# Performance work log

Hardware: AMD Instinct MI355X
Metric: run time of the kernel (lower is better)

## Reference

```python
import jax, jax.numpy as jnp
import numpy as np

NUM_HEADS = 4
KEY_DIM = 64
D_MODEL = 256
OUTPUT_DIM = 256


def setup_inputs() -> dict:
    key = jax.random.key(0)
    ks = jax.random.split(key, 11)
    B, T, D = 16, 1024, D_MODEL
    HD = NUM_HEADS * KEY_DIM
    s = 0.02
    return {
        "query": jax.random.normal(ks[0], (B, T, D), jnp.float32),
        "key": jax.random.normal(ks[1], (B, T, D), jnp.float32),
        "value": jax.random.normal(ks[2], (B, T, D), jnp.float32),
        "Wq": jax.random.normal(ks[3], (D, HD), jnp.float32) * s,
        "bq": jnp.zeros((HD,), jnp.float32),
        "Wk": jax.random.normal(ks[4], (D, HD), jnp.float32) * s,
        "bk": jnp.zeros((HD,), jnp.float32),
        "Wv": jax.random.normal(ks[5], (D, KEY_DIM), jnp.float32) * s,
        "bv": jnp.zeros((KEY_DIM,), jnp.float32),
        "Wo": jax.random.normal(ks[6], (HD, OUTPUT_DIM), jnp.float32) * s,
        "bo": jnp.zeros((OUTPUT_DIM,), jnp.float32),
    }


def reference(query, key, value, Wq, bq, Wk, bk, Wv, bv, Wo, bo):
    B, Tq, _ = query.shape
    Tk = key.shape[1]
    H, Dk = NUM_HEADS, KEY_DIM
    # projections
    q = (query @ Wq + bq).reshape(B, Tq, H, Dk)  # [B,Tq,H,Dk]
    k = (key @ Wk + bk).reshape(B, Tk, H, Dk)    # [B,Tk,H,Dk]
    v = value @ Wv + bv                           # [B,Tk,Dk] shared across heads
    scale = jnp.asarray(Dk, q.dtype) ** -0.5
    # scores [B,H,Tq,Tk]
    score = jnp.einsum("bqhd,bkhd->bhqk", q, k) * scale
    attn = jax.nn.softmax(score, axis=-1)
    # broadcast-V attention: [B,H,Tq,Tk] x [B,Tk,Dk] -> [B,H,Tq,Dk]
    out = jnp.einsum("bhqk,bkd->bhqd", attn, v)
    out = out.transpose(0, 2, 1, 3).reshape(B, Tq, H * Dk)
    return out @ Wo + bo
```

## Files before the change

### kernel.cpp

```cpp
#include <hip/hip_runtime.h>
#include <hip/hip_bf16.h>


typedef __attribute__((ext_vector_type(8))) short short8;
typedef __attribute__((ext_vector_type(4))) short s16x4;
typedef __attribute__((ext_vector_type(4))) float f32x4;

__device__ __forceinline__ short f2bf(float x) {
    return __builtin_bit_cast(short, __float2bfloat16(x));
}

__device__ __forceinline__ float exp2_fast(float x) {
#if __has_builtin(__builtin_amdgcn_exp2f)
    return __builtin_amdgcn_exp2f(x);
#else
    float r; asm("v_exp_f32 %0, %1" : "=v"(r) : "v"(x)); return r;
#endif
}

__device__ __forceinline__ f32x4 mfma16(short8 a, short8 b, f32x4 c) {
    return __builtin_amdgcn_mfma_f32_16x16x32_bf16(a, b, c, 0, 0, 0);
}
__device__ __forceinline__ f32x4 mfma16k16(s16x4 a, s16x4 b, f32x4 c) {
    return __builtin_amdgcn_mfma_f32_16x16x16bf16_1k(a, b, c, 0, 0, 0);
}

__device__ __forceinline__ void gll16(const float4* gsrc, float4* ldst) {
    __builtin_amdgcn_global_load_lds(
        (const __attribute__((address_space(1))) void*)gsrc,
        (__attribute__((address_space(3))) void*)ldst, 16, 0, 0);
}

#define QSCALE 0.18033688011112042f

__global__ void prep_weights(const float* __restrict__ Wq, const float* __restrict__ Wk,
                             const float* __restrict__ Wv, const float* __restrict__ Wo,
                             short* __restrict__ WqtF, short* __restrict__ WktF,
                             short* __restrict__ WvtF, short* __restrict__ WotF) {
    int tid = blockIdx.x * 256 + threadIdx.x;
    int n = tid >> 8, k = tid & 255;
    int off = ((n >> 6) << 14) + (((n >> 4) & 3) << 12) + ((k >> 5) << 9)
            + (((k >> 3) & 3) << 7) + ((n & 15) << 3) + (k & 7);
    WqtF[off] = f2bf(Wq[k * 256 + n] * QSCALE);
    WktF[off] = f2bf(Wk[k * 256 + n]);
    WotF[off] = f2bf(Wo[k * 256 + n]);
    if (n < 64) {
        int offv = ((n >> 4) << 12) + ((k >> 5) << 9) + (((k >> 3) & 3) << 7)
                 + ((n & 15) << 3) + (k & 7);
        WvtF[offv] = f2bf(Wv[k * 64 + n]);
    }
}

__global__ __launch_bounds__(256) void proj_all(
        const float* __restrict__ query, const float* __restrict__ key_,
        const float* __restrict__ value,
        const short* __restrict__ WqtF, const short* __restrict__ WktF,
        const short* __restrict__ WvtF,
        const float* __restrict__ bq, const float* __restrict__ bk,
        const float* __restrict__ bv,
        short* __restrict__ qf, short* __restrict__ kf, short* __restrict__ vf) {
    __shared__ short At[16384];
    const int tid = threadIdx.x;
    const int lane = tid & 63, wave = tid >> 6;
    const int u = lane >> 4, r16 = lane & 15;
    const int m0 = blockIdx.x * 64;
    const int task = blockIdx.y;

    const float* A = task == 0 ? query : (task == 1 ? key_ : value);

    #pragma unroll
    for (int j = 0; j < 8; ++j) {
        int p8 = j * 4 + u;
        int row = (wave << 4) + r16;
        const float* src = A + (m0 + row) * 256 + p8 * 8;
        float4 a0 = *(const float4*)src;
        float4 a1 = *(const float4*)(src + 4);
        short8 w;
        w[0] = f2bf(a0.x); w[1] = f2bf(a0.y); w[2] = f2bf(a0.z); w[3] = f2bf(a0.w);
        w[4] = f2bf(a1.x); w[5] = f2bf(a1.y); w[6] = f2bf(a1.z); w[7] = f2bf(a1.w);
        int dst = ((p8 >> 2) << 11) + (wave << 9) + ((p8 & 3) << 7) + (r16 << 3);
        *(short8*)&At[dst] = w;
    }
    __syncthreads();

    const int b = m0 >> 10, t64 = (m0 & 1023) >> 6;

    if (task < 2) {
        const short* WtF = task == 0 ? WqtF : WktF;
        const float* bias = task == 0 ? bq : bk;
        const float bscale = task == 0 ? QSCALE : 1.0f;
        short* outF = task == 0 ? qf : kf;

        f32x4 acc[4][4] = {};
        const short* wb = WtF + (wave << 14);
        #pragma unroll
        for (int kk = 0; kk < 8; ++kk) {
            short8 af[4], bf8[4];
            #pragma unroll
            for (int f = 0; f < 4; ++f) af[f] = *(const short8*)&At[(kk << 11) + (f << 9) + lane * 8];
            #pragma unroll
            for (int g = 0; g < 4; ++g) bf8[g] = *(const short8*)&wb[(g << 12) + (kk << 9) + lane * 8];
            #pragma unroll
            for (int f = 0; f < 4; ++f)
                #pragma unroll
                for (int g = 0; g < 4; ++g)
                    acc[f][g] = mfma16(af[f], bf8[g], acc[f][g]);
        }

        float bvv[4];
        #pragma unroll
        for (int g = 0; g < 4; ++g) bvv[g] = bias[(wave << 6) + 16 * g + r16] * bscale;
        short* ob = outF + ((((b << 2) + wave) << 4) + t64) * 4096;
        #pragma unroll
        for (int f = 0; f < 4; ++f)
            #pragma unroll
            for (int g = 0; g < 4; ++g) {
                int base = (f << 10) + ((g >> 1) << 9)
                         + (((2 * g + (r16 >> 3)) & 3) << 7) + (r16 & 7);
                #pragma unroll
                for (int rr = 0; rr < 4; ++rr)
                    ob[base + (4 * u + rr) * 8] = f2bf(acc[f][g][rr] + bvv[g]);
            }
    } else {
        f32x4 acc[4] = {};
        #pragma unroll
        for (int kk = 0; kk < 8; ++kk) {
            short8 af = *(const short8*)&At[(kk << 11) + (wave << 9) + lane * 8];
            #pragma unroll
            for (int g = 0; g < 4; ++g) {
                short8 bf8 = *(const short8*)&WvtF[(g << 12) + (kk << 9) + lane * 8];
                acc[g] = mfma16(af, bf8, acc[g]);
            }
        }
        short* ob = vf + ((b << 4) + t64) * 4096;
        #pragma unroll
        for (int dg = 0; dg < 4; ++dg) {
            float bvv = bv[16 * dg + r16];
            s16x4 o;
            #pragma unroll
            for (int rr = 0; rr < 4; ++rr) o[rr] = f2bf(acc[dg][rr] + bvv);
            *(s16x4*)&ob[(dg << 10) + ((wave >> 1) << 9) + lane * 8 + ((wave & 1) << 2)] = o;
        }
    }
}

__global__ __launch_bounds__(256) void attn_kernel(const short* __restrict__ qF,
        const short* __restrict__ kF, const short* __restrict__ vF,
        short* __restrict__ aoF) {
    __shared__ float4 Kt[2][512];
    __shared__ float4 Vt[2][512];
    const int tid = threadIdx.x;
    const int lane = tid & 63, wave = tid >> 6;
    const int u = lane >> 4, r16 = lane & 15;

    const int lin = blockIdx.x;
    const int L = (lin & 7) * 64 + (lin >> 3);
    const int qt2 = L & 7, h = (L >> 3) & 3, b = L >> 5;

    const short* qb = qF + ((((b << 2) + h) << 4) + 2 * qt2) * 4096 + (wave << 10);
    short8 qA0 = *(const short8*)&qb[lane * 8];
    short8 qA1 = *(const short8*)&qb[512 + lane * 8];
    short8 qB0 = *(const short8*)&qb[4096 + lane * 8];
    short8 qB1 = *(const short8*)&qb[4096 + 512 + lane * 8];

    const float4* kb = (const float4*)(kF + (((b << 2) + h) << 16));
    const float4* vb = (const float4*)(vF + (b << 16));

    #pragma unroll
    for (int j = 0; j < 4; ++j) {
        int ch = (wave << 2) + j;
        if (ch < 8) gll16(kb + (ch << 6) + lane, (float4*)Kt[0] + (ch << 6));
        else        gll16(vb + ((ch - 8) << 6) + lane, (float4*)Vt[0] + ((ch - 8) << 6));
    }
    asm volatile("s_waitcnt vmcnt(0)" ::: "memory");
    __syncthreads();

    f32x4 acc0[4] = {}, acc1[4] = {};
    f32x4 accl0 = {}, accl1 = {};
    s16x4 ones;
    { short o = (short)0x3F80; ones[0] = o; ones[1] = o; ones[2] = o; ones[3] = o; }

    for (int kt = 0; kt < 16; ++kt) {
        const int buf = kt & 1;
        if (kt < 15) {
            const float4* ks = kb + (kt + 1) * 512;
            const float4* vs = vb + (kt + 1) * 512;
            float4* kd = (float4*)Kt[buf ^ 1];
            float4* vd = (float4*)Vt[buf ^ 1];
            #pragma unroll
            for (int j = 0; j < 4; ++j) {
                int ch = (wave << 2) + j;
                if (ch < 8) gll16(ks + (ch << 6) + lane, kd + (ch << 6));
                else        gll16(vs + ((ch - 8) << 6) + lane, vd + ((ch - 8) << 6));
            }
        }

        const short* Kl = (const short*)Kt[buf];
        const short* Vl = (const short*)Vt[buf];

        f32x4 s0[4], s1[4];
        __builtin_amdgcn_s_setprio(1);
        #pragma unroll
        for (int g = 0; g < 4; ++g) {
            short8 k0 = *(const short8*)&Kl[(g << 10) + lane * 8];
            short8 k1 = *(const short8*)&Kl[(g << 10) + 512 + lane * 8];
            f32x4 z0 = {}, z1 = {};
            z0 = mfma16(k0, qA0, z0);
            s0[g] = mfma16(k1, qA1, z0);
            z1 = mfma16(k0, qB0, z1);
            s1[g] = mfma16(k1, qB1, z1);
        }
        __builtin_amdgcn_s_setprio(0);

        s16x4 pk0[4], pk1[4];
        #pragma unroll
        for (int g = 0; g < 4; ++g)
            #pragma unroll
            for (int rr = 0; rr < 4; ++rr) {
                pk0[g][rr] = f2bf(exp2_fast(s0[g][rr]));
                pk1[g][rr] = f2bf(exp2_fast(s1[g][rr]));
            }

        __builtin_amdgcn_s_setprio(1);
        #pragma unroll
        for (int g = 0; g < 4; ++g) {
            accl0 = mfma16k16(ones, pk0[g], accl0);
            accl1 = mfma16k16(ones, pk1[g], accl1);
        }
        #pragma unroll
        for (int dg = 0; dg < 4; ++dg) {
            #pragma unroll
            for (int gp = 0; gp < 2; ++gp) {
                short8 v8 = *(const short8*)&Vl[(dg << 10) + (gp << 9) + lane * 8];
                s16x4 vlo = { v8[0], v8[1], v8[2], v8[3] };
                s16x4 vhi = { v8[4], v8[5], v8[6], v8[7] };
                acc0[dg] = mfma16k16(vlo, pk0[2 * gp], acc0[dg]);
                acc0[dg] = mfma16k16(vhi, pk0[2 * gp + 1], acc0[dg]);
                acc1[dg] = mfma16k16(vlo, pk1[2 * gp], acc1[dg]);
                acc1[dg] = mfma16k16(vhi, pk1[2 * gp + 1], acc1[dg]);
            }
        }
        __builtin_amdgcn_s_setprio(0);

        asm volatile("s_waitcnt vmcnt(0)" ::: "memory");
        __syncthreads();
    }

    float li0 = 1.0f / accl0[0];
    float li1 = 1.0f / accl1[0];

    short* ob0 = aoF + (((b << 4) + 2 * qt2) << 14);
    #pragma unroll
    for (int dg = 0; dg < 4; ++dg) {
        int off = ((2 * h + (dg >> 1)) << 11) + (wave << 9)
                + (((2 * dg + (u >> 1)) & 3) << 7) + (r16 << 3) + ((u & 1) << 2);
        s16x4 o0, o1;
        #pragma unroll
        for (int rr = 0; rr < 4; ++rr) {
            o0[rr] = f2bf(acc0[dg][rr] * li0);
            o1[rr] = f2bf(acc1[dg][rr] * li1);
        }
        *(s16x4*)&ob0[off] = o0;
        *(s16x4*)&ob0[16384 + off] = o1;
    }
}

__global__ __launch_bounds__(256) void ogemm(const short* __restrict__ AF,
        const short* __restrict__ WoF, const float* __restrict__ bias,
        float* __restrict__ outp) {
    __shared__ short At[8192];
    const int tid = threadIdx.x;
    const int lane = tid & 63, wave = tid >> 6;
    const int u = lane >> 4, r16 = lane & 15;
    const int m0 = blockIdx.x * 32;
    const int mtile = m0 >> 6;
    const int fh = (m0 >> 4) & 2;

    const short* ab = AF + (mtile << 14) + (fh << 9);
    #pragma unroll
    for (int j = 0; j < 4; ++j) {
        int n = j * 256 + tid;
        int kk = n >> 7, rem = n & 127;
        *(short8*)&At[n * 8] = *(const short8*)&ab[(kk << 11) + rem * 8];
    }
    __syncthreads();

    f32x4 acc[2][4] = {};
    const short* wb = WoF + (wave << 14);
    #pragma unroll
    for (int kk = 0; kk < 8; ++kk) {
        short8 af[2], bf8[4];
        #pragma unroll
        for (int f = 0; f < 2; ++f) af[f] = *(const short8*)&At[(kk << 10) + (f << 9) + lane * 8];
        #pragma unroll
        for (int g = 0; g < 4; ++g) bf8[g] = *(const short8*)&wb[(g << 12) + (kk << 9) + lane * 8];
        #pragma unroll
        for (int f = 0; f < 2; ++f)
            #pragma unroll
            for (int g = 0; g < 4; ++g)
                acc[f][g] = mfma16(af[f], bf8[g], acc[f][g]);
    }

    float bvv[4];
    #pragma unroll
    for (int g = 0; g < 4; ++g) bvv[g] = bias[(wave << 6) + 16 * g + r16];
    #pragma unroll
    for (int f = 0; f < 2; ++f)
        #pragma unroll
        for (int g = 0; g < 4; ++g)
            #pragma unroll
            for (int rr = 0; rr < 4; ++rr)
                outp[(m0 + 16 * f + 4 * u + rr) * 256 + (wave << 6) + 16 * g + r16]
                    = acc[f][g][rr] + bvv[g];
}

extern "C" void kernel_launch(void* const* d_in, const int* in_sizes, int n_in,
                              void* d_out, int out_size, void* d_ws, size_t ws_size,
                              hipStream_t stream) {
    (void)in_sizes; (void)n_in; (void)out_size; (void)ws_size;
    const float* query = (const float*)d_in[0];
    const float* key_  = (const float*)d_in[1];
    const float* value = (const float*)d_in[2];
    const float* Wq = (const float*)d_in[3];
    const float* bq = (const float*)d_in[4];
    const float* Wk = (const float*)d_in[5];
    const float* bk = (const float*)d_in[6];
    const float* Wv = (const float*)d_in[7];
    const float* bv = (const float*)d_in[8];
    const float* Wo = (const float*)d_in[9];
    const float* bo = (const float*)d_in[10];
    float* outp = (float*)d_out;

    short* wsp  = (short*)d_ws;
    short* WqtF = wsp;
    short* WktF = wsp + 65536;
    short* WotF = wsp + 131072;
    short* WvtF = wsp + 196608;
    short* qf   = wsp + 212992;
    short* kf   = wsp + 4407296;
    short* vf   = wsp + 8601600;
    short* aof  = wsp + 9650176;

    hipLaunchKernelGGL(prep_weights, dim3(256), dim3(256), 0, stream,
                       Wq, Wk, Wv, Wo, WqtF, WktF, WvtF, WotF);
    hipLaunchKernelGGL(proj_all, dim3(256, 3), dim3(256), 0, stream,
                       query, key_, value, WqtF, WktF, WvtF, bq, bk, bv, qf, kf, vf);
    hipLaunchKernelGGL(attn_kernel, dim3(512), dim3(256), 0, stream, qf, kf, vf, aof);
    hipLaunchKernelGGL(ogemm, dim3(512), dim3(256), 0, stream, aof, WotF, bo, outp);
}
```

Before: 64.11 us.

## Triple-buffer attention K/V loads and software-pipeline weight fetches in GEMMs

```diff
diff --git a/kernel.cpp b/kernel.cpp
--- a/kernel.cpp
+++ b/kernel.cpp
@@ -59,52 +59,60 @@
         const float* __restrict__ bq, const float* __restrict__ bk,
         const float* __restrict__ bv,
         short* __restrict__ qf, short* __restrict__ kf, short* __restrict__ vf) {
-    __shared__ short At[16384];
+    __shared__ short At[8192];
     const int tid = threadIdx.x;
     const int lane = tid & 63, wave = tid >> 6;
     const int u = lane >> 4, r16 = lane & 15;
-    const int m0 = blockIdx.x * 64;
+    const int m0 = blockIdx.x * 32;
     const int task = blockIdx.y;
 
     const float* A = task == 0 ? query : (task == 1 ? key_ : value);
 
     #pragma unroll
-    for (int j = 0; j < 8; ++j) {
-        int p8 = j * 4 + u;
-        int row = (wave << 4) + r16;
+    for (int j = 0; j < 4; ++j) {
+        int p8 = j * 8 + ((wave >> 1) << 2) + u;
+        int row = ((wave & 1) << 4) + r16;
         const float* src = A + (m0 + row) * 256 + p8 * 8;
         float4 a0 = *(const float4*)src;
         float4 a1 = *(const float4*)(src + 4);
         short8 w;
         w[0] = f2bf(a0.x); w[1] = f2bf(a0.y); w[2] = f2bf(a0.z); w[3] = f2bf(a0.w);
         w[4] = f2bf(a1.x); w[5] = f2bf(a1.y); w[6] = f2bf(a1.z); w[7] = f2bf(a1.w);
-        int dst = ((p8 >> 2) << 11) + (wave << 9) + ((p8 & 3) << 7) + (r16 << 3);
+        int dst = ((p8 >> 2) << 10) + ((wave & 1) << 9) + ((p8 & 3) << 7) + (r16 << 3);
         *(short8*)&At[dst] = w;
     }
-    __syncthreads();
-
-    const int b = m0 >> 10, t64 = (m0 & 1023) >> 6;
+
+    const int b = m0 >> 10, t64 = (m0 & 1023) >> 6, half = (m0 >> 5) & 1;
 
     if (task < 2) {
         const short* WtF = task == 0 ? WqtF : WktF;
         const float* bias = task == 0 ? bq : bk;
         const float bscale = task == 0 ? QSCALE : 1.0f;
         short* outF = task == 0 ? qf : kf;
-
-        f32x4 acc[4][4] = {};
         const short* wb = WtF + (wave << 14);
+
+        short8 bf8[4];
+        #pragma unroll
+        for (int g = 0; g < 4; ++g) bf8[g] = *(const short8*)&wb[(g << 12) + lane * 8];
+        __syncthreads();
+
+        f32x4 acc[2][4] = {};
         #pragma unroll
         for (int kk = 0; kk < 8; ++kk) {
-            short8 af[4], bf8[4];
-            #pragma unroll
-            for (int f = 0; f < 4; ++f) af[f] = *(const short8*)&At[(kk << 11) + (f << 9) + lane * 8];
-            #pragma unroll
-            for (int g = 0; g < 4; ++g) bf8[g] = *(const short8*)&wb[(g << 12) + (kk << 9) + lane * 8];
-            #pragma unroll
-            for (int f = 0; f < 4; ++f)
+            short8 af[2], nb[4];
+            #pragma unroll
+            for (int f = 0; f < 2; ++f) af[f] = *(const short8*)&At[(kk << 10) + (f << 9) + lane * 8];
+            if (kk < 7) {
+                #pragma unroll
+                for (int g = 0; g < 4; ++g) nb[g] = *(const short8*)&wb[(g << 12) + ((kk + 1) << 9) + lane * 8];
+            }
+            #pragma unroll
+            for (int f = 0; f < 2; ++f)
                 #pragma unroll
                 for (int g = 0; g < 4; ++g)
                     acc[f][g] = mfma16(af[f], bf8[g], acc[f][g]);
+            #pragma unroll
+            for (int g = 0; g < 4; ++g) bf8[g] = nb[g];
         }
 
         float bvv[4];
@@ -112,34 +120,54 @@
         for (int g = 0; g < 4; ++g) bvv[g] = bias[(wave << 6) + 16 * g + r16] * bscale;
         short* ob = outF + ((((b << 2) + wave) << 4) + t64) * 4096;
         #pragma unroll
-        for (int f = 0; f < 4; ++f)
+        for (int f = 0; f < 2; ++f) {
+            int fg = half * 2 + f;
             #pragma unroll
             for (int g = 0; g < 4; ++g) {
-                int base = (f << 10) + ((g >> 1) << 9)
+                int base = (fg << 10) + ((g >> 1) << 9)
                          + (((2 * g + (r16 >> 3)) & 3) << 7) + (r16 & 7);
                 #pragma unroll
                 for (int rr = 0; rr < 4; ++rr)
                     ob[base + (4 * u + rr) * 8] = f2bf(acc[f][g][rr] + bvv[g]);
             }
+        }
     } else {
-        f32x4 acc[4] = {};
+        const int f = wave >> 1;
+        short8 bf8[2];
+        #pragma unroll
+        for (int z = 0; z < 2; ++z) {
+            int dg = ((wave & 1) << 1) + z;
+            bf8[z] = *(const short8*)&WvtF[(dg << 12) + lane * 8];
+        }
+        __syncthreads();
+
+        f32x4 acc[2] = {};
         #pragma unroll
         for (int kk = 0; kk < 8; ++kk) {
-            short8 af = *(const short8*)&At[(kk << 11) + (wave << 9) + lane * 8];
-            #pragma unroll
-            for (int g = 0; g < 4; ++g) {
-                short8 bf8 = *(const short8*)&WvtF[(g << 12) + (kk << 9) + lane * 8];
-                acc[g] = mfma16(af, bf8, acc[g]);
-            }
-        }
+            short8 af = *(const short8*)&At[(kk << 10) + (f << 9) + lane * 8];
+            short8 nb[2];
+            if (kk < 7) {
+                #pragma unroll
+                for (int z = 0; z < 2; ++z) {
+                    int dg = ((wave & 1) << 1) + z;
+                    nb[z] = *(const short8*)&WvtF[(dg << 12) + ((kk + 1) << 9) + lane * 8];
+                }
+            }
+            #pragma unroll
+            for (int z = 0; z < 2; ++z) acc[z] = mfma16(af, bf8[z], acc[z]);
+            bf8[0] = nb[0]; bf8[1] = nb[1];
+        }
+
         short* ob = vf + ((b << 4) + t64) * 4096;
-        #pragma unroll
-        for (int dg = 0; dg < 4; ++dg) {
+        const int gg = half * 2 + f;
+        #pragma unroll
+        for (int z = 0; z < 2; ++z) {
+            int dg = ((wave & 1) << 1) + z;
             float bvv = bv[16 * dg + r16];
             s16x4 o;
             #pragma unroll
-            for (int rr = 0; rr < 4; ++rr) o[rr] = f2bf(acc[dg][rr] + bvv);
-            *(s16x4*)&ob[(dg << 10) + ((wave >> 1) << 9) + lane * 8 + ((wave & 1) << 2)] = o;
+            for (int rr = 0; rr < 4; ++rr) o[rr] = f2bf(acc[z][rr] + bvv);
+            *(s16x4*)&ob[(dg << 10) + ((gg >> 1) << 9) + lane * 8 + ((gg & 1) << 2)] = o;
         }
     }
 }
@@ -147,8 +175,7 @@
 __global__ __launch_bounds__(256) void attn_kernel(const short* __restrict__ qF,
         const short* __restrict__ kF, const short* __restrict__ vF,
         short* __restrict__ aoF) {
-    __shared__ float4 Kt[2][512];
-    __shared__ float4 Vt[2][512];
+    __shared__ float4 KV[3][1024];
     const int tid = threadIdx.x;
     const int lane = tid & 63, wave = tid >> 6;
     const int u = lane >> 4, r16 = lane & 15;
@@ -166,37 +193,35 @@
     const float4* kb = (const float4*)(kF + (((b << 2) + h) << 16));
     const float4* vb = (const float4*)(vF + (b << 16));
 
-    #pragma unroll
-    for (int j = 0; j < 4; ++j) {
-        int ch = (wave << 2) + j;
-        if (ch < 8) gll16(kb + (ch << 6) + lane, (float4*)Kt[0] + (ch << 6));
-        else        gll16(vb + ((ch - 8) << 6) + lane, (float4*)Vt[0] + ((ch - 8) << 6));
-    }
-    asm volatile("s_waitcnt vmcnt(0)" ::: "memory");
-    __syncthreads();
+    #define STAGE(t, buf)                                                     \
+        {                                                                     \
+            const float4* ks_ = kb + (t) * 512;                               \
+            const float4* vs_ = vb + (t) * 512;                               \
+            _Pragma("unroll")                                                 \
+            for (int j_ = 0; j_ < 4; ++j_) {                                  \
+                int ch_ = (wave << 2) + j_;                                   \
+                if (ch_ < 8) gll16(ks_ + (ch_ << 6) + lane, &KV[buf][ch_ << 6]); \
+                else gll16(vs_ + ((ch_ - 8) << 6) + lane, &KV[buf][512 + ((ch_ - 8) << 6)]); \
+            }                                                                 \
+        }
+
+    STAGE(0, 0)
+    STAGE(1, 1)
+    asm volatile("s_waitcnt vmcnt(4)" ::: "memory");
+    __builtin_amdgcn_s_barrier();
 
     f32x4 acc0[4] = {}, acc1[4] = {};
     f32x4 accl0 = {}, accl1 = {};
     s16x4 ones;
     { short o = (short)0x3F80; ones[0] = o; ones[1] = o; ones[2] = o; ones[3] = o; }
 
+    #pragma unroll
     for (int kt = 0; kt < 16; ++kt) {
-        const int buf = kt & 1;
-        if (kt < 15) {
-            const float4* ks = kb + (kt + 1) * 512;
-            const float4* vs = vb + (kt + 1) * 512;
-            float4* kd = (float4*)Kt[buf ^ 1];
-            float4* vd = (float4*)Vt[buf ^ 1];
-            #pragma unroll
-            for (int j = 0; j < 4; ++j) {
-                int ch = (wave << 2) + j;
-                if (ch < 8) gll16(ks + (ch << 6) + lane, kd + (ch << 6));
-                else        gll16(vs + ((ch - 8) << 6) + lane, vd + ((ch - 8) << 6));
-            }
-        }
-
-        const short* Kl = (const short*)Kt[buf];
-        const short* Vl = (const short*)Vt[buf];
+        const int buf = kt % 3;
+        if (kt + 2 < 16) STAGE(kt + 2, (kt + 2) % 3)
+
+        const short* Kl = (const short*)&KV[buf][0];
+        const short* Vl = (const short*)&KV[buf][512];
 
         f32x4 s0[4], s1[4];
         __builtin_amdgcn_s_setprio(1);
@@ -242,8 +267,13 @@
         }
         __builtin_amdgcn_s_setprio(0);
 
-        asm volatile("s_waitcnt vmcnt(0)" ::: "memory");
-        __syncthreads();
+        if (kt < 14) {
+            asm volatile("s_waitcnt vmcnt(4)" ::: "memory");
+            __builtin_amdgcn_s_barrier();
+        } else if (kt < 15) {
+            asm volatile("s_waitcnt vmcnt(0)" ::: "memory");
+            __builtin_amdgcn_s_barrier();
+        }
     }
 
     float li0 = 1.0f / accl0[0];
@@ -263,6 +293,7 @@
         *(s16x4*)&ob0[off] = o0;
         *(s16x4*)&ob0[16384 + off] = o1;
     }
+    #undef STAGE
 }
 
 __global__ __launch_bounds__(256) void ogemm(const short* __restrict__ AF,
@@ -283,22 +314,30 @@
         int kk = n >> 7, rem = n & 127;
         *(short8*)&At[n * 8] = *(const short8*)&ab[(kk << 11) + rem * 8];
     }
+
+    const short* wb = WoF + (wave << 14);
+    short8 bf8[4];
+    #pragma unroll
+    for (int g = 0; g < 4; ++g) bf8[g] = *(const short8*)&wb[(g << 12) + lane * 8];
     __syncthreads();
 
     f32x4 acc[2][4] = {};
-    const short* wb = WoF + (wave << 14);
     #pragma unroll
     for (int kk = 0; kk < 8; ++kk) {
-        short8 af[2], bf8[4];
+        short8 af[2], nb[4];
         #pragma unroll
         for (int f = 0; f < 2; ++f) af[f] = *(const short8*)&At[(kk << 10) + (f << 9) + lane * 8];
-        #pragma unroll
-        for (int g = 0; g < 4; ++g) bf8[g] = *(const short8*)&wb[(g << 12) + (kk << 9) + lane * 8];
+        if (kk < 7) {
+            #pragma unroll
+            for (int g = 0; g < 4; ++g) nb[g] = *(const short8*)&wb[(g << 12) + ((kk + 1) << 9) + lane * 8];
+        }
         #pragma unroll
         for (int f = 0; f < 2; ++f)
             #pragma unroll
             for (int g = 0; g < 4; ++g)
                 acc[f][g] = mfma16(af[f], bf8[g], acc[f][g]);
+        #pragma unroll
+        for (int g = 0; g < 4; ++g) bf8[g] = nb[g];
     }
 
     float bvv[4];
@@ -343,7 +382,7 @@
 
     hipLaunchKernelGGL(prep_weights, dim3(256), dim3(256), 0, stream,
                        Wq, Wk, Wv, Wo, WqtF, WktF, WvtF, WotF);
-    hipLaunchKernelGGL(proj_all, dim3(256, 3), dim3(256), 0, stream,
+    hipLaunchKernelGGL(proj_all, dim3(512, 3), dim3(256), 0, stream,
                        query, key_, value, WqtF, WktF, WvtF, bq, bk, bv, qf, kf, vf);
     hipLaunchKernelGGL(attn_kernel, dim3(512), dim3(256), 0, stream, qf, kf, vf, aof);
     hipLaunchKernelGGL(ogemm, dim3(512), dim3(256), 0, stream, aof, WotF, bo, outp);
```

Result: faster. 62.47 us (-2.6%).
